# Performance work log

Hardware: AMD Instinct MI355X
Metric: run time of the kernel (lower is better)

Reference implementation:

```python
import jax, jax.numpy as jnp
import numpy as np

EPS = 1e-9
KERNEL = 3


def kernel_tile(x, kernel, stride):
    """im2col-style patch extraction. x: [B,H,W,...] -> [B,OH,OW,kernel*kernel,depth]."""
    B, H, W = x.shape[:3]
    depth = int(np.prod(x.shape[3:]))
    x = x.reshape(B, H, W, depth)
    OH = (H - kernel) // stride + 1
    OW = (W - kernel) // stride + 1
    patches = jnp.stack(
        [x[:, i:i + (OH - 1) * stride + 1:stride, j:j + (OW - 1) * stride + 1:stride, :]
         for i in range(kernel) for j in range(kernel)], axis=3)
    return patches  # [B,OH,OW,k*k,depth]


def em_routing(votes, i_act, beta_v, beta_a, routings):
    # votes: [B,S,S,I,O,16], i_act: [B,S,S,I], beta_*: [1,1,1,O]
    I, O = votes.shape[-3], votes.shape[-2]
    rr = jnp.full((I, O, 1), 1.0 / O, dtype=votes.dtype)
    i_act = i_act[..., None, None]           # [B,S,S,I,1,1]
    bv = beta_v[..., None, :, None]          # [1,1,1,1,O,1]
    ba = beta_a[..., None, :, None]
    it_min, it_max = 1.0, min(float(routings), 3.0)
    o_mean = o_act = None
    for it in range(routings):
        inv_temp = it_min + (it_max - it_min) * it / max(1.0, routings - 1.0)
        # M-step
        rr_prime = rr * i_act                                        # [B,S,S,I,O,1]
        rr_sum = jnp.sum(rr_prime, axis=-3, keepdims=True)           # [B,S,S,1,O,1]
        o_mean = jnp.sum(rr_prime * votes, axis=-3, keepdims=True) / rr_sum  # [B,S,S,1,O,16]
        o_stdv = jnp.sqrt(jnp.sum(rr_prime * jnp.square(votes - o_mean), axis=-3, keepdims=True) / rr_sum)
        o_cost = (bv + jnp.log(o_stdv + EPS)) * rr_sum               # [B,S,S,1,O,16]
        o_act = jax.nn.sigmoid(inv_temp * (ba - jnp.sum(o_cost, axis=-1, keepdims=True)))  # [B,S,S,1,O,1]
        if it < routings - 1:
            # E-step: log Gaussian prob of each vote under each output capsule
            o_p = (-jnp.sum(jnp.square(votes - o_mean) / (2.0 * jnp.square(o_stdv)), axis=-1, keepdims=True)
                   - jnp.sum(jnp.log(o_stdv + EPS), axis=-1, keepdims=True))  # [B,S,S,I,O,1]
            zz = jnp.log(o_act + EPS) + o_p
            rr = jax.nn.softmax(zz, axis=-2)                          # softmax over O
    pose = jnp.squeeze(o_mean, axis=-3)      # [B,S,S,O,16]
    act = jnp.squeeze(o_act, axis=(-3, -1))  # [B,S,S,O]
    return pose, act


def setup_inputs() -> dict:
    key = jax.random.key(0)
    ks = jax.random.split(key, 5)
    B, H, W, I_SIZE, O_SIZE = 4, 14, 14, 32, 32
    inputs_pose = jax.random.normal(ks[0], (B, H, W, I_SIZE, 4, 4), dtype=jnp.float32)
    inputs_activation = jax.random.uniform(ks[1], (B, H, W, I_SIZE), dtype=jnp.float32)
    w = jax.random.normal(ks[2], (1, 3 * 3 * I_SIZE, O_SIZE, 4, 4), dtype=jnp.float32)
    beta_v = 0.1 * jax.random.normal(ks[3], (1, 1, 1, O_SIZE), dtype=jnp.float32)
    beta_a = 0.1 * jax.random.normal(ks[4], (1, 1, 1, O_SIZE), dtype=jnp.float32)
    return {"inputs_pose": inputs_pose, "inputs_activation": inputs_activation,
            "w": w, "beta_v": beta_v, "beta_a": beta_a, "stride": 1, "routings": 3}


def reference(inputs_pose, inputs_activation, w, beta_v, beta_a, stride, routings):
    B = inputs_pose.shape[0]
    pose_size = inputs_pose.shape[-1]            # 4
    i_size = inputs_pose.shape[3]
    o_size = w.shape[2]
    tp = kernel_tile(inputs_pose, KERNEL, stride)        # [B,S,S,9,i*16]
    ta = kernel_tile(inputs_activation, KERNEL, stride)  # [B,S,S,9,i]
    S = ta.shape[1]
    I = KERNEL * KERNEL * i_size
    poses = tp.reshape(-1, I, pose_size, pose_size)      # [N,I,4,4], N = B*S*S
    acts = ta.reshape(B, S, S, I)
    # vote transform: per (input capsule, output capsule) 4x4 matmul
    votes = jnp.einsum('nipq,ioqr->niopr', poses, w[0])  # [N,I,O,4,4]
    votes = votes.reshape(B, S, S, I, o_size, pose_size * pose_size)
    pose, activation = em_routing(votes, acts, beta_v, beta_a, routings)
    pose = pose.reshape(B, S, S, o_size, pose_size, pose_size)
    return pose, activation
```

## Files before the change

kernel.cpp:

```cpp
#include <hip/hip_runtime.h>
#include <math.h>

namespace {

constexpr int BATCH = 4;
constexpr int H_IN  = 14;
constexpr int W_IN  = 14;
constexpr int ICAP  = 32;
constexpr int OCAP  = 32;
constexpr int SOUT  = 12;
constexpr int NI    = 288;
constexpr int PD    = 16;
constexpr float EPSF = 1e-9f;

__global__ __launch_bounds__(256, 2)
void caps_em_kernel(const float* __restrict__ pose_in,
                    const float* __restrict__ act_in,
                    const float* __restrict__ wmat,
                    const float* __restrict__ beta_v,
                    const float* __restrict__ beta_a,
                    float* __restrict__ out)
{
    __shared__ __align__(16) float sP[NI][PD];
    __shared__ float sA[NI];
    __shared__ float sMean[OCAP][PD + 1];
    __shared__ float sInv2[OCAP][PD + 1];
    __shared__ float sLogSigSum[OCAP];
    __shared__ float sLogAct[OCAP];
    __shared__ float sOAct[OCAP];
    __shared__ float sS0[OCAP];
    __shared__ float sRedS[4][OCAP][2 * PD + 1];
    __shared__ float sRed0[4][OCAP];

    const int n  = blockIdx.x;
    const int b  = n / (SOUT * SOUT);
    const int yx = n % (SOUT * SOUT);
    const int y  = yx / SOUT;
    const int x  = yx % SOUT;

    const int t    = threadIdx.x;
    const int lane = t & 63;
    const int wave = t >> 6;
    const int o    = lane & 31;
    const int half = lane >> 5;

    for (int k = 0; k < 9; ++k) {
        const int ki = k / 3, kj = k % 3;
        const int cell = (b * H_IN + (y + ki)) * W_IN + (x + kj);
        const float2* srcp = reinterpret_cast<const float2*>(pose_in + (size_t)cell * (ICAP * PD));
        float2* dst = reinterpret_cast<float2*>(&sP[k * ICAP][0]);
        dst[t] = srcp[t];
        if (t < ICAP) sA[k * ICAP + t] = act_in[(size_t)cell * ICAP + t];
    }
    __syncthreads();

    for (int sweep = 0; sweep < 3; ++sweep) {
        float s1[PD], s2[PD];
        float s0 = 0.f;
        #pragma unroll
        for (int d = 0; d < PD; ++d) { s1[d] = 0.f; s2[d] = 0.f; }

        for (int step = 0; step < NI / 8; ++step) {
            const int i = step * 8 + wave * 2 + half;

            float P[PD], W[PD];
            #pragma unroll
            for (int q4 = 0; q4 < 4; ++q4) {
                const float4 pv = *reinterpret_cast<const float4*>(&sP[i][q4 * 4]);
                P[q4*4+0] = pv.x; P[q4*4+1] = pv.y; P[q4*4+2] = pv.z; P[q4*4+3] = pv.w;
            }
            const float* wr = wmat + ((size_t)i * OCAP + o) * PD;
            #pragma unroll
            for (int q4 = 0; q4 < 4; ++q4) {
                const float4 wv = *reinterpret_cast<const float4*>(&wr[q4 * 4]);
                W[q4*4+0] = wv.x; W[q4*4+1] = wv.y; W[q4*4+2] = wv.z; W[q4*4+3] = wv.w;
            }
            float v[PD];
            #pragma unroll
            for (int p = 0; p < 4; ++p) {
                #pragma unroll
                for (int r = 0; r < 4; ++r) {
                    float acc = P[p*4+0] * W[r];
                    acc = fmaf(P[p*4+1], W[4+r],  acc);
                    acc = fmaf(P[p*4+2], W[8+r],  acc);
                    acc = fmaf(P[p*4+3], W[12+r], acc);
                    v[p*4+r] = acc;
                }
            }

            float rrp;
            if (sweep == 0) {
                rrp = sA[i] * (1.0f / 32.0f);
            } else {
                float ts = 0.f;
                #pragma unroll
                for (int d = 0; d < PD; ++d) {
                    const float diff = v[d] - sMean[o][d];
                    ts = fmaf(diff * diff, sInv2[o][d], ts);
                }
                float zz = sLogAct[o] - ts - sLogSigSum[o];
                float m = zz;
                #pragma unroll
                for (int msk = 16; msk >= 1; msk >>= 1)
                    m = fmaxf(m, __shfl_xor(m, msk, 32));
                const float e = __expf(zz - m);
                float es = e;
                #pragma unroll
                for (int msk = 16; msk >= 1; msk >>= 1)
                    es += __shfl_xor(es, msk, 32);
                rrp = (e / es) * sA[i];
            }

            s0 += rrp;
            #pragma unroll
            for (int d = 0; d < PD; ++d) {
                s1[d] = fmaf(rrp, v[d], s1[d]);
                s2[d] = fmaf(rrp * v[d], v[d], s2[d]);
            }
        }

        #pragma unroll
        for (int d = 0; d < PD; ++d) {
            s1[d] += __shfl_xor(s1[d], 32, 64);
            s2[d] += __shfl_xor(s2[d], 32, 64);
        }
        s0 += __shfl_xor(s0, 32, 64);

        if (half == 0) {
            #pragma unroll
            for (int d = 0; d < PD; ++d) {
                sRedS[wave][o][d]      = s1[d];
                sRedS[wave][o][PD + d] = s2[d];
            }
            sRed0[wave][o] = s0;
        }
        __syncthreads();

        if (t < OCAP)
            sS0[t] = sRed0[0][t] + sRed0[1][t] + sRed0[2][t] + sRed0[3][t];
        __syncthreads();

        {
            const int oo    = t >> 3;
            const int dbase = (t & 7) * 2;
            const float s0t    = sS0[oo];
            const float inv_s0 = 1.0f / s0t;
            float lsum = 0.f;
            float meanv[2];
            #pragma unroll
            for (int j = 0; j < 2; ++j) {
                const int d = dbase + j;
                const float S1t = sRedS[0][oo][d] + sRedS[1][oo][d]
                                + sRedS[2][oo][d] + sRedS[3][oo][d];
                const float S2t = sRedS[0][oo][PD+d] + sRedS[1][oo][PD+d]
                                + sRedS[2][oo][PD+d] + sRedS[3][oo][PD+d];
                const float mean = S1t * inv_s0;
                float var = fmaf(-mean, mean, S2t * inv_s0);
                var = fmaxf(var, 0.f);
                const float sig = sqrtf(var);
                lsum += __logf(sig + EPSF);
                sMean[oo][d] = mean;
                sInv2[oo][d] = 0.5f / fmaxf(var, 1e-30f);
                meanv[j] = mean;
            }
            float ltot = lsum;
            ltot += __shfl_xor(ltot, 1, 8);
            ltot += __shfl_xor(ltot, 2, 8);
            ltot += __shfl_xor(ltot, 4, 8);
            if ((t & 7) == 0) {
                sLogSigSum[oo] = ltot;
                const float cost    = s0t * fmaf(16.f, beta_v[oo], ltot);
                const float invtemp = 1.0f + (float)sweep;
                const float zact    = invtemp * (beta_a[oo] - cost);
                const float oact    = 1.0f / (1.0f + __expf(-zact));
                sOAct[oo]   = oact;
                sLogAct[oo] = __logf(oact + EPSF);
            }
            if (sweep == 2) {
                float* outp = out + (size_t)n * (OCAP * PD);
                outp[oo * PD + dbase]     = meanv[0];
                outp[oo * PD + dbase + 1] = meanv[1];
            }
        }
        __syncthreads();
        if (sweep == 2 && t < OCAP)
            out[(size_t)BATCH * SOUT * SOUT * OCAP * PD + (size_t)n * OCAP + t] = sOAct[t];
    }
}

}

extern "C" void kernel_launch(void* const* d_in, const int* in_sizes, int n_in,
                              void* d_out, int out_size, void* d_ws, size_t ws_size,
                              hipStream_t stream) {
    const float* pose_in = (const float*)d_in[0];
    const float* act_in  = (const float*)d_in[1];
    const float* wmat    = (const float*)d_in[2];
    const float* beta_v  = (const float*)d_in[3];
    const float* beta_a  = (const float*)d_in[4];
    float* out = (float*)d_out;

    dim3 grid(BATCH * SOUT * SOUT);
    dim3 block(256);
    caps_em_kernel<<<grid, block, 0, stream>>>(pose_in, act_in, wmat, beta_v, beta_a, out);
}
```

Baseline: 119.1 us.

## Split EM routing into per-sweep kernels with input-capsule partitioning across blocks

The single kernel, which ran one block per output position through all three routing sweeps, is replaced by three templated sweep kernels plus a final kernel. Each sweep splits the 288 input capsules across 4 blocks per position, giving 4x more blocks. Partial sufficient statistics go to a workspace and the next launch reduces them. Poses are now read directly from global memory instead of being staged in shared memory. This raises parallelism and occupancy on a small grid, at the cost of extra launches, workspace traffic and repeated global pose loads.

```diff
diff --git a/kernel.cpp b/kernel.cpp
--- a/kernel.cpp
+++ b/kernel.cpp
@@ -3,188 +3,211 @@
 
 namespace {
 
-constexpr int BATCH = 4;
-constexpr int H_IN  = 14;
-constexpr int W_IN  = 14;
-constexpr int ICAP  = 32;
-constexpr int OCAP  = 32;
-constexpr int SOUT  = 12;
-constexpr int NI    = 288;
-constexpr int PD    = 16;
+constexpr int SOUT = 12;
+constexpr int OCAP = 32;
+constexpr int PD   = 16;
+constexpr int NI   = 288;
+constexpr int SUBS = 4;
+constexpr int ISUB = NI / SUBS;
+constexpr int NPOS = 4 * SOUT * SOUT;
 constexpr float EPSF = 1e-9f;
-
-__global__ __launch_bounds__(256, 2)
-void caps_em_kernel(const float* __restrict__ pose_in,
-                    const float* __restrict__ act_in,
-                    const float* __restrict__ wmat,
-                    const float* __restrict__ beta_v,
-                    const float* __restrict__ beta_a,
-                    float* __restrict__ out)
+constexpr int CHUNK = 33 * 32;
+constexpr size_t POSE_OUT = (size_t)NPOS * OCAP * PD;
+
+template<int SWEEP>
+__global__ __launch_bounds__(256, 4)
+void sweep_kernel(const float* __restrict__ pose_in,
+                  const float* __restrict__ act_in,
+                  const float* __restrict__ wmat,
+                  const float* __restrict__ beta_v,
+                  const float* __restrict__ beta_a,
+                  const float* __restrict__ prev,
+                  float* __restrict__ outbuf)
 {
-    __shared__ __align__(16) float sP[NI][PD];
-    __shared__ float sA[NI];
     __shared__ float sMean[OCAP][PD + 1];
     __shared__ float sInv2[OCAP][PD + 1];
-    __shared__ float sLogSigSum[OCAP];
-    __shared__ float sLogAct[OCAP];
-    __shared__ float sOAct[OCAP];
-    __shared__ float sS0[OCAP];
-    __shared__ float sRedS[4][OCAP][2 * PD + 1];
-    __shared__ float sRed0[4][OCAP];
-
-    const int n  = blockIdx.x;
-    const int b  = n / (SOUT * SOUT);
-    const int yx = n % (SOUT * SOUT);
-    const int y  = yx / SOUT;
-    const int x  = yx % SOUT;
+    __shared__ float sBias[OCAP];
+    __shared__ float sRed[4][33][OCAP];
+
+    const int bid = blockIdx.x;
+    const int n   = bid >> 2;
+    const int sub = bid & 3;
+    const int b   = n / (SOUT * SOUT);
+    const int yx  = n % (SOUT * SOUT);
+    const int y   = yx / SOUT;
+    const int x   = yx % SOUT;
 
     const int t    = threadIdx.x;
+    const int wave = t >> 6;
     const int lane = t & 63;
-    const int wave = t >> 6;
     const int o    = lane & 31;
     const int half = lane >> 5;
 
-    for (int k = 0; k < 9; ++k) {
-        const int ki = k / 3, kj = k % 3;
-        const int cell = (b * H_IN + (y + ki)) * W_IN + (x + kj);
-        const float2* srcp = reinterpret_cast<const float2*>(pose_in + (size_t)cell * (ICAP * PD));
-        float2* dst = reinterpret_cast<float2*>(&sP[k * ICAP][0]);
-        dst[t] = srcp[t];
-        if (t < ICAP) sA[k * ICAP + t] = act_in[(size_t)cell * ICAP + t];
+    if constexpr (SWEEP > 0) {
+        const int oo = t >> 3, dp = t & 7, d0 = dp * 2;
+        const float* base = prev + (size_t)n * (SUBS * CHUNK);
+        float s0 = 0.f, S1a = 0.f, S1b = 0.f, S2a = 0.f, S2b = 0.f;
+        #pragma unroll
+        for (int s = 0; s < SUBS; ++s) {
+            const float* c = base + s * CHUNK;
+            s0  += c[32 * 32 + oo];
+            S1a += c[(d0)      * 32 + oo];
+            S1b += c[(d0 + 1)  * 32 + oo];
+            S2a += c[(16 + d0) * 32 + oo];
+            S2b += c[(17 + d0) * 32 + oo];
+        }
+        const float inv = 1.f / s0;
+        const float m0 = S1a * inv, m1 = S1b * inv;
+        const float v0 = fmaxf(fmaf(-m0, m0, S2a * inv), 0.f);
+        const float v1 = fmaxf(fmaf(-m1, m1, S2b * inv), 0.f);
+        const float lsum = __logf(sqrtf(v0) + EPSF) + __logf(sqrtf(v1) + EPSF);
+        sMean[oo][d0] = m0;  sMean[oo][d0 + 1] = m1;
+        sInv2[oo][d0] = 0.5f / fmaxf(v0, 1e-30f);
+        sInv2[oo][d0 + 1] = 0.5f / fmaxf(v1, 1e-30f);
+        float lt = lsum;
+        lt += __shfl_xor(lt, 1, 8);
+        lt += __shfl_xor(lt, 2, 8);
+        lt += __shfl_xor(lt, 4, 8);
+        if (dp == 0) {
+            const float cost    = s0 * fmaf(16.f, beta_v[oo], lt);
+            const float invtemp = (float)SWEEP;
+            const float oact    = 1.f / (1.f + __expf(-invtemp * (beta_a[oo] - cost)));
+            sBias[oo] = __logf(oact + EPSF) - lt;
+        }
+        __syncthreads();
+    }
+
+    float s1[PD], s2[PD];
+    float s0acc = 0.f;
+    #pragma unroll
+    for (int d = 0; d < PD; ++d) { s1[d] = 0.f; s2[d] = 0.f; }
+
+    #pragma unroll 1
+    for (int step = 0; step < ISUB / 8; ++step) {
+        const int i  = sub * ISUB + step * 8 + wave * 2 + half;
+        const int k  = i >> 5;
+        const int c  = i & 31;
+        const int ki = k / 3, kj = k - ki * 3;
+        const int cell = (b * 14 + y + ki) * 14 + (x + kj);
+
+        const float* pr = pose_in + ((size_t)cell * 32 + c) * PD;
+        const float a_i = act_in[(size_t)cell * 32 + c];
+        float P[PD], W[PD];
+        #pragma unroll
+        for (int q4 = 0; q4 < 4; ++q4) {
+            const float4 pv = *reinterpret_cast<const float4*>(&pr[q4 * 4]);
+            P[q4*4+0] = pv.x; P[q4*4+1] = pv.y; P[q4*4+2] = pv.z; P[q4*4+3] = pv.w;
+        }
+        const float* wr = wmat + ((size_t)i * OCAP + o) * PD;
+        #pragma unroll
+        for (int q4 = 0; q4 < 4; ++q4) {
+            const float4 wv = *reinterpret_cast<const float4*>(&wr[q4 * 4]);
+            W[q4*4+0] = wv.x; W[q4*4+1] = wv.y; W[q4*4+2] = wv.z; W[q4*4+3] = wv.w;
+        }
+
+        float v[PD];
+        #pragma unroll
+        for (int p = 0; p < 4; ++p) {
+            #pragma unroll
+            for (int r = 0; r < 4; ++r) {
+                float acc = P[p*4+0] * W[r];
+                acc = fmaf(P[p*4+1], W[4  + r], acc);
+                acc = fmaf(P[p*4+2], W[8  + r], acc);
+                acc = fmaf(P[p*4+3], W[12 + r], acc);
+                v[p*4+r] = acc;
+            }
+        }
+
+        float rrp;
+        if constexpr (SWEEP == 0) {
+            rrp = a_i * (1.0f / 32.0f);
+        } else {
+            float ts = 0.f;
+            #pragma unroll
+            for (int d = 0; d < PD; ++d) {
+                const float diff = v[d] - sMean[o][d];
+                ts = fmaf(diff * diff, sInv2[o][d], ts);
+            }
+            float zz = sBias[o] - ts;
+            float m = zz;
+            #pragma unroll
+            for (int msk = 16; msk >= 1; msk >>= 1)
+                m = fmaxf(m, __shfl_xor(m, msk, 32));
+            const float e = __expf(zz - m);
+            float es = e;
+            #pragma unroll
+            for (int msk = 16; msk >= 1; msk >>= 1)
+                es += __shfl_xor(es, msk, 32);
+            rrp = (e / es) * a_i;
+        }
+
+        s0acc += rrp;
+        #pragma unroll
+        for (int d = 0; d < PD; ++d) {
+            const float rv = rrp * v[d];
+            s1[d] = fmaf(rrp, v[d], s1[d]);
+            s2[d] = fmaf(rv, v[d], s2[d]);
+        }
+    }
+
+    #pragma unroll
+    for (int d = 0; d < PD; ++d) {
+        s1[d] += __shfl_xor(s1[d], 32, 64);
+        s2[d] += __shfl_xor(s2[d], 32, 64);
+    }
+    s0acc += __shfl_xor(s0acc, 32, 64);
+
+    if (half == 0) {
+        #pragma unroll
+        for (int d = 0; d < PD; ++d) {
+            sRed[wave][d][o]      = s1[d];
+            sRed[wave][16 + d][o] = s2[d];
+        }
+        sRed[wave][32][o] = s0acc;
     }
     __syncthreads();
 
-    for (int sweep = 0; sweep < 3; ++sweep) {
-        float s1[PD], s2[PD];
-        float s0 = 0.f;
-        #pragma unroll
-        for (int d = 0; d < PD; ++d) { s1[d] = 0.f; s2[d] = 0.f; }
-
-        for (int step = 0; step < NI / 8; ++step) {
-            const int i = step * 8 + wave * 2 + half;
-
-            float P[PD], W[PD];
-            #pragma unroll
-            for (int q4 = 0; q4 < 4; ++q4) {
-                const float4 pv = *reinterpret_cast<const float4*>(&sP[i][q4 * 4]);
-                P[q4*4+0] = pv.x; P[q4*4+1] = pv.y; P[q4*4+2] = pv.z; P[q4*4+3] = pv.w;
-            }
-            const float* wr = wmat + ((size_t)i * OCAP + o) * PD;
-            #pragma unroll
-            for (int q4 = 0; q4 < 4; ++q4) {
-                const float4 wv = *reinterpret_cast<const float4*>(&wr[q4 * 4]);
-                W[q4*4+0] = wv.x; W[q4*4+1] = wv.y; W[q4*4+2] = wv.z; W[q4*4+3] = wv.w;
-            }
-            float v[PD];
-            #pragma unroll
-            for (int p = 0; p < 4; ++p) {
-                #pragma unroll
-                for (int r = 0; r < 4; ++r) {
-                    float acc = P[p*4+0] * W[r];
-                    acc = fmaf(P[p*4+1], W[4+r],  acc);
-                    acc = fmaf(P[p*4+2], W[8+r],  acc);
-                    acc = fmaf(P[p*4+3], W[12+r], acc);
-                    v[p*4+r] = acc;
-                }
-            }
-
-            float rrp;
-            if (sweep == 0) {
-                rrp = sA[i] * (1.0f / 32.0f);
-            } else {
-                float ts = 0.f;
-                #pragma unroll
-                for (int d = 0; d < PD; ++d) {
-                    const float diff = v[d] - sMean[o][d];
-                    ts = fmaf(diff * diff, sInv2[o][d], ts);
-                }
-                float zz = sLogAct[o] - ts - sLogSigSum[o];
-                float m = zz;
-                #pragma unroll
-                for (int msk = 16; msk >= 1; msk >>= 1)
-                    m = fmaxf(m, __shfl_xor(m, msk, 32));
-                const float e = __expf(zz - m);
-                float es = e;
-                #pragma unroll
-                for (int msk = 16; msk >= 1; msk >>= 1)
-                    es += __shfl_xor(es, msk, 32);
-                rrp = (e / es) * sA[i];
-            }
-
-            s0 += rrp;
-            #pragma unroll
-            for (int d = 0; d < PD; ++d) {
-                s1[d] = fmaf(rrp, v[d], s1[d]);
-                s2[d] = fmaf(rrp * v[d], v[d], s2[d]);
-            }
-        }
-
-        #pragma unroll
-        for (int d = 0; d < PD; ++d) {
-            s1[d] += __shfl_xor(s1[d], 32, 64);
-            s2[d] += __shfl_xor(s2[d], 32, 64);
-        }
-        s0 += __shfl_xor(s0, 32, 64);
-
-        if (half == 0) {
-            #pragma unroll
-            for (int d = 0; d < PD; ++d) {
-                sRedS[wave][o][d]      = s1[d];
-                sRedS[wave][o][PD + d] = s2[d];
-            }
-            sRed0[wave][o] = s0;
-        }
-        __syncthreads();
-
-        if (t < OCAP)
-            sS0[t] = sRed0[0][t] + sRed0[1][t] + sRed0[2][t] + sRed0[3][t];
-        __syncthreads();
-
-        {
-            const int oo    = t >> 3;
-            const int dbase = (t & 7) * 2;
-            const float s0t    = sS0[oo];
-            const float inv_s0 = 1.0f / s0t;
-            float lsum = 0.f;
-            float meanv[2];
-            #pragma unroll
-            for (int j = 0; j < 2; ++j) {
-                const int d = dbase + j;
-                const float S1t = sRedS[0][oo][d] + sRedS[1][oo][d]
-                                + sRedS[2][oo][d] + sRedS[3][oo][d];
-                const float S2t = sRedS[0][oo][PD+d] + sRedS[1][oo][PD+d]
-                                + sRedS[2][oo][PD+d] + sRedS[3][oo][PD+d];
-                const float mean = S1t * inv_s0;
-                float var = fmaf(-mean, mean, S2t * inv_s0);
-                var = fmaxf(var, 0.f);
-                const float sig = sqrtf(var);
-                lsum += __logf(sig + EPSF);
-                sMean[oo][d] = mean;
-                sInv2[oo][d] = 0.5f / fmaxf(var, 1e-30f);
-                meanv[j] = mean;
-            }
-            float ltot = lsum;
-            ltot += __shfl_xor(ltot, 1, 8);
-            ltot += __shfl_xor(ltot, 2, 8);
-            ltot += __shfl_xor(ltot, 4, 8);
-            if ((t & 7) == 0) {
-                sLogSigSum[oo] = ltot;
-                const float cost    = s0t * fmaf(16.f, beta_v[oo], ltot);
-                const float invtemp = 1.0f + (float)sweep;
-                const float zact    = invtemp * (beta_a[oo] - cost);
-                const float oact    = 1.0f / (1.0f + __expf(-zact));
-                sOAct[oo]   = oact;
-                sLogAct[oo] = __logf(oact + EPSF);
-            }
-            if (sweep == 2) {
-                float* outp = out + (size_t)n * (OCAP * PD);
-                outp[oo * PD + dbase]     = meanv[0];
-                outp[oo * PD + dbase + 1] = meanv[1];
-            }
-        }
-        __syncthreads();
-        if (sweep == 2 && t < OCAP)
-            out[(size_t)BATCH * SOUT * SOUT * OCAP * PD + (size_t)n * OCAP + t] = sOAct[t];
+    float* dst = outbuf + (size_t)bid * CHUNK;
+    const int oc = t & 31;
+    for (int j = t >> 5; j < 33; j += 8)
+        dst[j * 32 + oc] = sRed[0][j][oc] + sRed[1][j][oc] + sRed[2][j][oc] + sRed[3][j][oc];
+}
+
+__global__ __launch_bounds__(256, 4)
+void final_kernel(const float* __restrict__ prev,
+                  const float* __restrict__ beta_v,
+                  const float* __restrict__ beta_a,
+                  float* __restrict__ out)
+{
+    const int n  = blockIdx.x;
+    const int t  = threadIdx.x;
+    const int oo = t >> 3, dp = t & 7, d0 = dp * 2;
+    const float* base = prev + (size_t)n * (SUBS * CHUNK);
+    float s0 = 0.f, S1a = 0.f, S1b = 0.f, S2a = 0.f, S2b = 0.f;
+    #pragma unroll
+    for (int s = 0; s < SUBS; ++s) {
+        const float* c = base + s * CHUNK;
+        s0  += c[32 * 32 + oo];
+        S1a += c[(d0)      * 32 + oo];
+        S1b += c[(d0 + 1)  * 32 + oo];
+        S2a += c[(16 + d0) * 32 + oo];
+        S2b += c[(17 + d0) * 32 + oo];
+    }
+    const float inv = 1.f / s0;
+    const float m0 = S1a * inv, m1 = S1b * inv;
+    out[(size_t)n * (OCAP * PD) + oo * PD + d0]     = m0;
+    out[(size_t)n * (OCAP * PD) + oo * PD + d0 + 1] = m1;
+
+    const float v0 = fmaxf(fmaf(-m0, m0, S2a * inv), 0.f);
+    const float v1 = fmaxf(fmaf(-m1, m1, S2b * inv), 0.f);
+    float lt = __logf(sqrtf(v0) + EPSF) + __logf(sqrtf(v1) + EPSF);
+    lt += __shfl_xor(lt, 1, 8);
+    lt += __shfl_xor(lt, 2, 8);
+    lt += __shfl_xor(lt, 4, 8);
+    if (dp == 0) {
+        const float cost = s0 * fmaf(16.f, beta_v[oo], lt);
+        const float oact = 1.f / (1.f + __expf(-3.0f * (beta_a[oo] - cost)));
+        out[POSE_OUT + (size_t)n * OCAP + oo] = oact;
     }
 }
 
@@ -200,7 +223,15 @@
     const float* beta_a  = (const float*)d_in[4];
     float* out = (float*)d_out;
 
-    dim3 grid(BATCH * SOUT * SOUT);
+    float* bufA = (float*)d_ws;
+    float* bufB = bufA + (size_t)NPOS * SUBS * CHUNK;
+
     dim3 block(256);
-    caps_em_kernel<<<grid, block, 0, stream>>>(pose_in, act_in, wmat, beta_v, beta_a, out);
-}
+    dim3 gridS(NPOS * SUBS);
+    dim3 gridF(NPOS);
+
+    sweep_kernel<0><<<gridS, block, 0, stream>>>(pose_in, act_in, wmat, beta_v, beta_a, nullptr, bufA);
+    sweep_kernel<1><<<gridS, block, 0, stream>>>(pose_in, act_in, wmat, beta_v, beta_a, bufA, bufB);
+    sweep_kernel<2><<<gridS, block, 0, stream>>>(pose_in, act_in, wmat, beta_v, beta_a, bufB, bufA);
+    final_kernel<<<gridF, block, 0, stream>>>(bufA, beta_v, beta_a, out);
+}
```

Result: slower. 138.0 us (+15.9%).

## Double block to 512 threads and expand Gaussian exponent into precomputed bias terms

Applied to the files above, without the earlier changes.

Each block now runs 8 waves over the 288 input capsules instead of 4, which halves the serial routing loop per thread. Partial sums are combined in two stages through a transposed shared buffer. The E-step squared-distance is expanded algebraically so that per-output constants (log activation, log sigma sum, mean^2/2var) fold into one bias, and per-element work becomes two FMAs with precomputed -2*mean*inv2 terms. The exact divide becomes __fdividef. The expanded form can lose precision through cancellation, and the larger block raises register and occupancy pressure.

```diff
diff --git a/kernel.cpp b/kernel.cpp
--- a/kernel.cpp
+++ b/kernel.cpp
@@ -3,34 +3,28 @@
 
 namespace {
 
-constexpr int BATCH = 4;
-constexpr int H_IN  = 14;
-constexpr int W_IN  = 14;
-constexpr int ICAP  = 32;
-constexpr int OCAP  = 32;
-constexpr int SOUT  = 12;
-constexpr int NI    = 288;
-constexpr int PD    = 16;
+constexpr int SOUT = 12;
+constexpr int OCAP = 32;
+constexpr int PD   = 16;
+constexpr int NI   = 288;
+constexpr int NPOS = 4 * SOUT * SOUT;
 constexpr float EPSF = 1e-9f;
-
-__global__ __launch_bounds__(256, 2)
-void caps_em_kernel(const float* __restrict__ pose_in,
-                    const float* __restrict__ act_in,
-                    const float* __restrict__ wmat,
-                    const float* __restrict__ beta_v,
-                    const float* __restrict__ beta_a,
-                    float* __restrict__ out)
+constexpr size_t POSE_OUT = (size_t)NPOS * OCAP * PD;
+
+__global__ __launch_bounds__(512, 6)
+void caps_em_fused(const float* __restrict__ pose_in,
+                   const float* __restrict__ act_in,
+                   const float* __restrict__ wmat,
+                   const float* __restrict__ beta_v,
+                   const float* __restrict__ beta_a,
+                   float* __restrict__ out)
 {
-    __shared__ __align__(16) float sP[NI][PD];
+    __shared__ __align__(16) float sP[NI * PD];
     __shared__ float sA[NI];
-    __shared__ float sMean[OCAP][PD + 1];
     __shared__ float sInv2[OCAP][PD + 1];
-    __shared__ float sLogSigSum[OCAP];
-    __shared__ float sLogAct[OCAP];
-    __shared__ float sOAct[OCAP];
-    __shared__ float sS0[OCAP];
-    __shared__ float sRedS[4][OCAP][2 * PD + 1];
-    __shared__ float sRed0[4][OCAP];
+    __shared__ float sNeg[OCAP][PD + 1];
+    __shared__ float sBias[OCAP];
+    __shared__ float sRed[4][33][33];
 
     const int n  = blockIdx.x;
     const int b  = n / (SOUT * SOUT);
@@ -39,34 +33,46 @@
     const int x  = yx % SOUT;
 
     const int t    = threadIdx.x;
+    const int wave = t >> 6;
     const int lane = t & 63;
-    const int wave = t >> 6;
     const int o    = lane & 31;
     const int half = lane >> 5;
 
-    for (int k = 0; k < 9; ++k) {
-        const int ki = k / 3, kj = k % 3;
-        const int cell = (b * H_IN + (y + ki)) * W_IN + (x + kj);
-        const float2* srcp = reinterpret_cast<const float2*>(pose_in + (size_t)cell * (ICAP * PD));
-        float2* dst = reinterpret_cast<float2*>(&sP[k * ICAP][0]);
-        dst[t] = srcp[t];
-        if (t < ICAP) sA[k * ICAP + t] = act_in[(size_t)cell * ICAP + t];
+    {
+        const float4* src = reinterpret_cast<const float4*>(pose_in);
+        float4* dst = reinterpret_cast<float4*>(sP);
+        for (int u = t; u < NI * 4; u += 512) {
+            const int k = u >> 7, idx = u & 127;
+            const int ki = k / 3, kj = k - ki * 3;
+            const int cell = (b * 14 + y + ki) * 14 + (x + kj);
+            dst[u] = src[(size_t)cell * 128 + idx];
+        }
+        for (int u = t; u < NI; u += 512) {
+            const int k = u >> 5, c = u & 31;
+            const int ki = k / 3, kj = k - ki * 3;
+            const int cell = (b * 14 + y + ki) * 14 + (x + kj);
+            sA[u] = act_in[(size_t)cell * 32 + c];
+        }
     }
     __syncthreads();
 
     for (int sweep = 0; sweep < 3; ++sweep) {
+        const float bias_r = (sweep > 0) ? sBias[o] : 0.f;
+
         float s1[PD], s2[PD];
         float s0 = 0.f;
         #pragma unroll
         for (int d = 0; d < PD; ++d) { s1[d] = 0.f; s2[d] = 0.f; }
 
-        for (int step = 0; step < NI / 8; ++step) {
-            const int i = step * 8 + wave * 2 + half;
+        #pragma unroll 1
+        for (int step = 0; step < NI / 16; ++step) {
+            const int i = step * 16 + wave * 2 + half;
 
             float P[PD], W[PD];
+            const float* pr = &sP[i * PD];
             #pragma unroll
             for (int q4 = 0; q4 < 4; ++q4) {
-                const float4 pv = *reinterpret_cast<const float4*>(&sP[i][q4 * 4]);
+                const float4 pv = *reinterpret_cast<const float4*>(&pr[q4 * 4]);
                 P[q4*4+0] = pv.x; P[q4*4+1] = pv.y; P[q4*4+2] = pv.z; P[q4*4+3] = pv.w;
             }
             const float* wr = wmat + ((size_t)i * OCAP + o) * PD;
@@ -75,30 +81,32 @@
                 const float4 wv = *reinterpret_cast<const float4*>(&wr[q4 * 4]);
                 W[q4*4+0] = wv.x; W[q4*4+1] = wv.y; W[q4*4+2] = wv.z; W[q4*4+3] = wv.w;
             }
+
             float v[PD];
             #pragma unroll
             for (int p = 0; p < 4; ++p) {
                 #pragma unroll
                 for (int r = 0; r < 4; ++r) {
                     float acc = P[p*4+0] * W[r];
-                    acc = fmaf(P[p*4+1], W[4+r],  acc);
-                    acc = fmaf(P[p*4+2], W[8+r],  acc);
-                    acc = fmaf(P[p*4+3], W[12+r], acc);
+                    acc = fmaf(P[p*4+1], W[4  + r], acc);
+                    acc = fmaf(P[p*4+2], W[8  + r], acc);
+                    acc = fmaf(P[p*4+3], W[12 + r], acc);
                     v[p*4+r] = acc;
                 }
             }
 
+            const float a_i = sA[i];
             float rrp;
             if (sweep == 0) {
-                rrp = sA[i] * (1.0f / 32.0f);
+                rrp = a_i * (1.0f / 32.0f);
             } else {
                 float ts = 0.f;
                 #pragma unroll
                 for (int d = 0; d < PD; ++d) {
-                    const float diff = v[d] - sMean[o][d];
-                    ts = fmaf(diff * diff, sInv2[o][d], ts);
+                    const float h = fmaf(v[d], sInv2[o][d], sNeg[o][d]);
+                    ts = fmaf(v[d], h, ts);
                 }
-                float zz = sLogAct[o] - ts - sLogSigSum[o];
+                float zz = bias_r - ts;
                 float m = zz;
                 #pragma unroll
                 for (int msk = 16; msk >= 1; msk >>= 1)
@@ -108,14 +116,15 @@
                 #pragma unroll
                 for (int msk = 16; msk >= 1; msk >>= 1)
                     es += __shfl_xor(es, msk, 32);
-                rrp = (e / es) * sA[i];
+                rrp = __fdividef(e, es) * a_i;
             }
 
             s0 += rrp;
             #pragma unroll
             for (int d = 0; d < PD; ++d) {
+                const float rv = rrp * v[d];
                 s1[d] = fmaf(rrp, v[d], s1[d]);
-                s2[d] = fmaf(rrp * v[d], v[d], s2[d]);
+                s2[d] = fmaf(rv, v[d], s2[d]);
             }
         }
 
@@ -126,65 +135,71 @@
         }
         s0 += __shfl_xor(s0, 32, 64);
 
-        if (half == 0) {
+        if (wave < 4 && half == 0) {
             #pragma unroll
             for (int d = 0; d < PD; ++d) {
-                sRedS[wave][o][d]      = s1[d];
-                sRedS[wave][o][PD + d] = s2[d];
-            }
-            sRed0[wave][o] = s0;
+                sRed[wave][d][o]      = s1[d];
+                sRed[wave][16 + d][o] = s2[d];
+            }
+            sRed[wave][32][o] = s0;
         }
         __syncthreads();
-
-        if (t < OCAP)
-            sS0[t] = sRed0[0][t] + sRed0[1][t] + sRed0[2][t] + sRed0[3][t];
+        if (wave >= 4 && half == 0) {
+            #pragma unroll
+            for (int d = 0; d < PD; ++d) {
+                sRed[wave - 4][d][o]      += s1[d];
+                sRed[wave - 4][16 + d][o] += s2[d];
+            }
+            sRed[wave - 4][32][o] += s0;
+        }
         __syncthreads();
 
-        {
-            const int oo    = t >> 3;
-            const int dbase = (t & 7) * 2;
-            const float s0t    = sS0[oo];
-            const float inv_s0 = 1.0f / s0t;
-            float lsum = 0.f;
-            float meanv[2];
-            #pragma unroll
-            for (int j = 0; j < 2; ++j) {
-                const int d = dbase + j;
-                const float S1t = sRedS[0][oo][d] + sRedS[1][oo][d]
-                                + sRedS[2][oo][d] + sRedS[3][oo][d];
-                const float S2t = sRedS[0][oo][PD+d] + sRedS[1][oo][PD+d]
-                                + sRedS[2][oo][PD+d] + sRedS[3][oo][PD+d];
-                const float mean = S1t * inv_s0;
-                float var = fmaf(-mean, mean, S2t * inv_s0);
-                var = fmaxf(var, 0.f);
-                const float sig = sqrtf(var);
-                lsum += __logf(sig + EPSF);
-                sMean[oo][d] = mean;
-                sInv2[oo][d] = 0.5f / fmaxf(var, 1e-30f);
-                meanv[j] = mean;
-            }
-            float ltot = lsum;
-            ltot += __shfl_xor(ltot, 1, 8);
-            ltot += __shfl_xor(ltot, 2, 8);
-            ltot += __shfl_xor(ltot, 4, 8);
-            if ((t & 7) == 0) {
-                sLogSigSum[oo] = ltot;
-                const float cost    = s0t * fmaf(16.f, beta_v[oo], ltot);
+        if (t < 256) {
+            const int oo = t >> 3, dp = t & 7, d0 = dp * 2;
+            float S0 = 0.f, S1a = 0.f, S1b = 0.f, S2a = 0.f, S2b = 0.f;
+            #pragma unroll
+            for (int r = 0; r < 4; ++r) {
+                S0  += sRed[r][32][oo];
+                S1a += sRed[r][d0][oo];
+                S1b += sRed[r][d0 + 1][oo];
+                S2a += sRed[r][16 + d0][oo];
+                S2b += sRed[r][17 + d0][oo];
+            }
+            const float inv = 1.f / S0;
+            const float m0 = S1a * inv, m1 = S1b * inv;
+            const float v0 = fmaxf(fmaf(-m0, m0, S2a * inv), 0.f);
+            const float v1 = fmaxf(fmaf(-m1, m1, S2b * inv), 0.f);
+            if (sweep == 2) {
+                float2 pv; pv.x = m0; pv.y = m1;
+                *reinterpret_cast<float2*>(out + (size_t)n * (OCAP * PD) + oo * PD + d0) = pv;
+            }
+            const float i20 = 0.5f / fmaxf(v0, 1e-30f);
+            const float i21 = 0.5f / fmaxf(v1, 1e-30f);
+            float llocal = __logf(sqrtf(v0) + EPSF) + __logf(sqrtf(v1) + EPSF);
+            float c0l    = m0 * m0 * i20 + m1 * m1 * i21;
+            if (sweep < 2) {
+                sInv2[oo][d0]     = i20;
+                sInv2[oo][d0 + 1] = i21;
+                sNeg[oo][d0]      = -2.f * m0 * i20;
+                sNeg[oo][d0 + 1]  = -2.f * m1 * i21;
+            }
+            #pragma unroll
+            for (int msk = 1; msk <= 4; msk <<= 1) {
+                llocal += __shfl_xor(llocal, msk, 8);
+                c0l    += __shfl_xor(c0l,    msk, 8);
+            }
+            if (dp == 0) {
+                const float lt   = llocal;
+                const float cost = S0 * fmaf(16.f, beta_v[oo], lt);
                 const float invtemp = 1.0f + (float)sweep;
-                const float zact    = invtemp * (beta_a[oo] - cost);
-                const float oact    = 1.0f / (1.0f + __expf(-zact));
-                sOAct[oo]   = oact;
-                sLogAct[oo] = __logf(oact + EPSF);
-            }
-            if (sweep == 2) {
-                float* outp = out + (size_t)n * (OCAP * PD);
-                outp[oo * PD + dbase]     = meanv[0];
-                outp[oo * PD + dbase + 1] = meanv[1];
+                const float oact = 1.f / (1.f + __expf(-invtemp * (beta_a[oo] - cost)));
+                if (sweep < 2)
+                    sBias[oo] = __logf(oact + EPSF) - lt - c0l;
+                else
+                    out[POSE_OUT + (size_t)n * OCAP + oo] = oact;
             }
         }
         __syncthreads();
-        if (sweep == 2 && t < OCAP)
-            out[(size_t)BATCH * SOUT * SOUT * OCAP * PD + (size_t)n * OCAP + t] = sOAct[t];
     }
 }
 
@@ -200,7 +215,6 @@
     const float* beta_a  = (const float*)d_in[4];
     float* out = (float*)d_out;
 
-    dim3 grid(BATCH * SOUT * SOUT);
-    dim3 block(256);
-    caps_em_kernel<<<grid, block, 0, stream>>>(pose_in, act_in, wmat, beta_v, beta_a, out);
+    caps_em_fused<<<dim3(NPOS), dim3(512), 0, stream>>>(
+        pose_in, act_in, wmat, beta_v, beta_a, out);
 }
```

Measured after the change: 152.8 us. 1.28x slower.
